# Performance work log

Measured on AMD Instinct MI355X. Metric: run time of the kernel, lower is better.

Reference implementation:

```python
import jax, jax.numpy as jnp
import numpy as np

N = 50000
E = 800000
IN_CH = 256
OUT_CH = 64   # per-head channels (PyG out_channels)
HEADS = 4
NEG_SLOPE = 0.2


def setup_inputs() -> dict:
    key = jax.random.key(0)
    k = jax.random.split(key, 8)
    x = jax.random.normal(k[0], (N, IN_CH), dtype=jnp.float32)
    edge_index = jax.random.randint(k[1], (2, E), 0, N, dtype=jnp.int64)
    # GATConv parameters
    W = jax.random.normal(k[2], (IN_CH, HEADS * OUT_CH), dtype=jnp.float32) * (1.0 / np.sqrt(IN_CH))
    att_src = jax.random.normal(k[3], (HEADS, OUT_CH), dtype=jnp.float32) * 0.1
    att_dst = jax.random.normal(k[4], (HEADS, OUT_CH), dtype=jnp.float32) * 0.1
    bias = jnp.zeros((OUT_CH,), dtype=jnp.float32)
    # residual linear (bias=False)
    W_res = jax.random.normal(k[5], (IN_CH, OUT_CH), dtype=jnp.float32) * (1.0 / np.sqrt(IN_CH))
    return {"x": x, "edge_index": edge_index, "W": W, "att_src": att_src,
            "att_dst": att_dst, "bias": bias, "W_res": W_res}


def _gat_forward(x, edge_index, W, att_src, att_dst, bias, W_res):
    # residual branch
    x_res = x @ W_res                                   # [N, OUT_CH]

    # node transform: [N, H, C]
    xw = (x @ W).reshape(N, HEADS, OUT_CH)
    # per-node attention logits, [N, H]
    a_src = jnp.einsum('nhc,hc->nh', xw, att_src)
    a_dst = jnp.einsum('nhc,hc->nh', xw, att_dst)

    # add self-loops (PyG GATConv default add_self_loops=True)
    loops = jnp.arange(N, dtype=edge_index.dtype)
    src = jnp.concatenate([edge_index[0], loops])       # [E+N]
    dst = jnp.concatenate([edge_index[1], loops])       # [E+N]

    # per-edge logits + leaky relu, [E+N, H]
    alpha = jax.nn.leaky_relu(a_src[src] + a_dst[dst], NEG_SLOPE)

    # segment softmax over destination nodes
    m = jax.ops.segment_max(alpha, dst, num_segments=N)    # [N, H]
    e = jnp.exp(alpha - m[dst])
    denom = jax.ops.segment_sum(e, dst, num_segments=N)    # [N, H]
    a = e / denom[dst]                                     # [E+N, H]
    # (dropout p=0.1 on attention coeffs is identity in eval mode)

    # weighted scatter-aggregate: [N, H, C]
    msgs = xw[src] * a[:, :, None]
    out = jax.ops.segment_sum(msgs, dst, num_segments=N)

    # concat=False -> mean over heads, then bias
    x_conv = out.mean(axis=1) + bias                     # [N, OUT_CH]
    return jax.nn.relu(x_conv + x_res)


def reference(x, edge_index, W, att_src, att_dst, bias, W_res):
    return _gat_forward(x, edge_index, W, att_src, att_dst, bias, W_res)
```

## Files before the change

### kernel.cpp

```cpp
#include <hip/hip_runtime.h>
#include <math.h>

#define N_NODES 50000
#define N_EDGES 800000
#define IN_CH   256
#define OUT_CH  64
#define HEADS   4
#define NEG_SLOPE 0.2f
#define NCOLS   320
#define NTILES  20
#define NKK     8
#define PACK_BLOCKS 40
#define GEMM_BLOCKS 782
#define SCAN_BLOCKS 196
#define NBINS   391
#define P1_BLOCKS 256
#define EPB     3125
#define AGG_BLOCKS 12500

typedef __attribute__((ext_vector_type(8))) short short8;
typedef __attribute__((ext_vector_type(4))) float f32x4;

__device__ __forceinline__ float lrelu(float v) {
    return v > 0.f ? v : NEG_SLOPE * v;
}
__device__ __forceinline__ unsigned bf16_rne(float f) {
    unsigned u = __float_as_uint(f);
    return (u + 0x7FFFu + ((u >> 16) & 1u)) >> 16;
}
__device__ __forceinline__ unsigned pack2(float lo, float hi) {
    return bf16_rne(lo) | (bf16_rne(hi) << 16);
}
__device__ __forceinline__ float bflo(unsigned u) { return __uint_as_float(u << 16); }
__device__ __forceinline__ float bfhi(unsigned u) { return __uint_as_float(u & 0xFFFF0000u); }
__device__ __forceinline__ short8 as_short8(uint4 u) {
    union { uint4 u4; short8 s8; } cv; cv.u4 = u; return cv.s8;
}

__global__ __launch_bounds__(256) void pack_B(
    const float* __restrict__ W, const float* __restrict__ Wres,
    uint4* __restrict__ Bp)
{
    const int idx  = blockIdx.x * 256 + threadIdx.x;
    const int kk   = idx / (NTILES * 64);
    const int rem  = idx - kk * (NTILES * 64);
    const int t    = rem >> 6;
    const int lane = rem & 63;
    const int colL = lane & 15, quad = lane >> 4;
    const int col  = t * 16 + colL;
    const int k0   = kk * 32 + quad * 8;
    float v[8];
    #pragma unroll
    for (int j = 0; j < 8; ++j) {
        const int k = k0 + j;
        v[j] = (col < IN_CH) ? W[(size_t)k * IN_CH + col]
                             : Wres[(size_t)k * OUT_CH + (col - IN_CH)];
    }
    uint4 u;
    u.x = pack2(v[0], v[1]); u.y = pack2(v[2], v[3]);
    u.z = pack2(v[4], v[5]); u.w = pack2(v[6], v[7]);
    Bp[(kk * NTILES + t) * 64 + lane] = u;
}

__global__ __launch_bounds__(256) void gemm_hist(
    const float* __restrict__ x, const uint4* __restrict__ Bp,
    uint2* __restrict__ xw2, float* __restrict__ xres,
    const int* __restrict__ ei, int* __restrict__ M,
    const float* __restrict__ attS, const float* __restrict__ attD,
    float* __restrict__ asrc, float* __restrict__ adst)
{
    __shared__ uint4 Alds[4 * NKK * 64];
    __shared__ float logS[64][HEADS];
    __shared__ float logD[64][HEADS];

    if (blockIdx.x >= GEMM_BLOCKS) {
        const int blk = blockIdx.x - GEMM_BLOCKS;
        int* lh = (int*)Alds;
        for (int b = threadIdx.x; b < NBINS; b += 256) lh[b] = 0;
        __syncthreads();
        const int e0 = blk * EPB;
        #pragma unroll
        for (int r = 0; r < 13; ++r) {
            const int idx = (r << 8) + threadIdx.x;
            if (idx < EPB)
                atomicAdd(&lh[ei[N_EDGES + e0 + idx] >> 7], 1);
        }
        __syncthreads();
        for (int b = threadIdx.x; b < NBINS; b += 256)
            M[(size_t)b * P1_BLOCKS + blk] = lh[b];
        return;
    }

    const int tid = threadIdx.x;
    const int n0  = blockIdx.x * 64;

    logS[tid >> 2][tid & 3] = 0.f;
    logD[tid >> 2][tid & 3] = 0.f;

    #pragma unroll
    for (int i = 0; i < 8; ++i) {
        const int e    = i * 256 + tid;
        const int g    = e >> 9;
        const int kk   = (e >> 6) & 7;
        const int lane = e & 63;
        const int cL   = lane & 15, qd = lane >> 4;
        const int row  = n0 + g * 16 + cL;
        const int k0   = kk * 32 + qd * 8;
        uint4 u = make_uint4(0u, 0u, 0u, 0u);
        if (row < N_NODES) {
            const float4 a = *reinterpret_cast<const float4*>(x + (size_t)row * IN_CH + k0);
            const float4 b = *reinterpret_cast<const float4*>(x + (size_t)row * IN_CH + k0 + 4);
            u.x = pack2(a.x, a.y); u.y = pack2(a.z, a.w);
            u.z = pack2(b.x, b.y); u.w = pack2(b.z, b.w);
        }
        Alds[(g * NKK + kk) * 64 + lane] = u;
    }
    __syncthreads();

    const int lane = tid & 63;
    const int wv   = tid >> 6;
    const int colL = lane & 15, quad = lane >> 4;

    f32x4 acc[4][5];
    #pragma unroll
    for (int rg = 0; rg < 4; ++rg)
        #pragma unroll
        for (int j = 0; j < 5; ++j) acc[rg][j] = (f32x4){0.f, 0.f, 0.f, 0.f};

    for (int kk = 0; kk < NKK; ++kk) {
        uint4 bu[5];
        #pragma unroll
        for (int j = 0; j < 5; ++j)
            bu[j] = Bp[(kk * NTILES + j * 4 + wv) * 64 + lane];
        #pragma unroll
        for (int rg = 0; rg < 4; ++rg) {
            const short8 a = as_short8(Alds[(rg * NKK + kk) * 64 + lane]);
            #pragma unroll
            for (int j = 0; j < 5; ++j)
                acc[rg][j] = __builtin_amdgcn_mfma_f32_16x16x32_bf16(
                    a, as_short8(bu[j]), acc[rg][j], 0, 0, 0);
        }
    }

    #pragma unroll
    for (int rg = 0; rg < 4; ++rg) {
        #pragma unroll
        for (int r = 0; r < 4; ++r) {
            const int row = n0 + rg * 16 + quad * 4 + r;
            if (row < N_NODES) {
                xw2[(size_t)row * 64 + wv * 16 + colL] = make_uint2(
                    pack2(acc[rg][0][r], acc[rg][1][r]),
                    pack2(acc[rg][2][r], acc[rg][3][r]));
                xres[(size_t)row * OUT_CH + wv * 16 + colL] = acc[rg][4][r];
            }
        }
    }

    float aSr[HEADS], aDr[HEADS];
    #pragma unroll
    for (int h = 0; h < HEADS; ++h) {
        aSr[h] = attS[h * 64 + wv * 16 + colL];
        aDr[h] = attD[h * 64 + wv * 16 + colL];
    }
    #pragma unroll
    for (int rg = 0; rg < 4; ++rg) {
        #pragma unroll
        for (int h = 0; h < HEADS; ++h) {
            #pragma unroll
            for (int r = 0; r < 4; ++r) {
                float vS = acc[rg][h][r] * aSr[h];
                float vD = acc[rg][h][r] * aDr[h];
                #pragma unroll
                for (int m = 1; m < 16; m <<= 1) {
                    vS += __shfl_xor(vS, m);
                    vD += __shfl_xor(vD, m);
                }
                if (colL == 0) {
                    atomicAdd(&logS[rg * 16 + quad * 4 + r][h], vS);
                    atomicAdd(&logD[rg * 16 + quad * 4 + r][h], vD);
                }
            }
        }
    }
    __syncthreads();
    {
        const int rl = tid >> 2, h = tid & 3;
        const int row = n0 + rl;
        if (row < N_NODES) {
            asrc[(size_t)row * HEADS + h] = logS[rl][h];
            adst[(size_t)row * HEADS + h] = logD[rl][h];
        }
    }
}

__global__ __launch_bounds__(256) void binscan_M(
    int* __restrict__ M, int* __restrict__ binCnt)
{
    __shared__ int ws[4];
    const int t = threadIdx.x, lane = t & 63, w = t >> 6;
    const int b = blockIdx.x;
    const int v = M[(size_t)b * P1_BLOCKS + t];
    int sc = v;
    #pragma unroll
    for (int off = 1; off < 64; off <<= 1) {
        const int n = __shfl_up(sc, off);
        if (lane >= off) sc += n;
    }
    if (lane == 63) ws[w] = sc;
    __syncthreads();
    int prefix = 0;
    for (int j = 0; j < w; ++j) prefix += ws[j];
    M[(size_t)b * P1_BLOCKS + t] = prefix + sc - v;
    if (t == 255) binCnt[b] = prefix + sc;
}

__global__ __launch_bounds__(512) void binstart_scan(
    const int* __restrict__ binCnt, int* __restrict__ binStart)
{
    __shared__ int ws[8];
    const int t = threadIdx.x, lane = t & 63, w = t >> 6;
    const int v = (t < NBINS) ? binCnt[t] : 0;
    int sc = v;
    #pragma unroll
    for (int off = 1; off < 64; off <<= 1) {
        const int n = __shfl_up(sc, off);
        if (lane >= off) sc += n;
    }
    if (lane == 63) ws[w] = sc;
    __syncthreads();
    int prefix = 0;
    for (int j = 0; j < w; ++j) prefix += ws[j];
    if (t < NBINS) binStart[t] = prefix + sc - v;
}

__global__ __launch_bounds__(256) void part_mid(
    const int* __restrict__ ei, const int* __restrict__ M,
    const int* __restrict__ binStart, unsigned* __restrict__ mid)
{
    __shared__ int baseL[NBINS];
    __shared__ int lh[NBINS];
    const int blk = blockIdx.x;
    for (int b = threadIdx.x; b < NBINS; b += 256) {
        baseL[b] = binStart[b] + M[(size_t)b * P1_BLOCKS + blk];
        lh[b] = 0;
    }
    __syncthreads();
    const int e0 = blk * EPB;
    #pragma unroll
    for (int r = 0; r < 13; ++r) {
        const int idx = (r << 8) + threadIdx.x;
        if (idx < EPB) {
            const int e = e0 + idx;
            const int d = ei[N_EDGES + e];
            const int b = d >> 7;
            const int pos = atomicAdd(&lh[b], 1);
            mid[baseL[b] + pos] = ((unsigned)(d & 127) << 17) | (unsigned)ei[e];
        }
    }
}

__global__ __launch_bounds__(256) void count_fine(
    const unsigned* __restrict__ mid, const int* __restrict__ binStart,
    const int* __restrict__ binCnt, int* __restrict__ cnt)
{
    __shared__ int c128[128];
    const int t = threadIdx.x, b = blockIdx.x;
    if (t < 128) c128[t] = 0;
    __syncthreads();
    const int base = binStart[b], n = binCnt[b];
    for (int i = t; i < n; i += 256)
        atomicAdd(&c128[mid[base + i] >> 17], 1);
    __syncthreads();
    if (t < 128) {
        const int d = (b << 7) + t;
        if (d < N_NODES) cnt[d] = c128[t];
    }
}

__global__ __launch_bounds__(256) void scan_local(
    const int* __restrict__ cnt, int* __restrict__ lscan, int* __restrict__ bsum)
{
    __shared__ int ws[4];
    const int t = threadIdx.x, lane = t & 63, w = t >> 6;
    const int i = blockIdx.x * 256 + t;
    const int v = (i < N_NODES) ? cnt[i] : 0;
    int sc = v;
    #pragma unroll
    for (int off = 1; off < 64; off <<= 1) {
        const int n = __shfl_up(sc, off);
        if (lane >= off) sc += n;
    }
    if (lane == 63) ws[w] = sc;
    __syncthreads();
    int prefix = 0;
    for (int j = 0; j < w; ++j) prefix += ws[j];
    if (i < N_NODES) lscan[i] = prefix + sc - v;
    if (t == 255) bsum[blockIdx.x] = prefix + sc;
}

__global__ __launch_bounds__(256) void scatter_fine(
    const unsigned* __restrict__ mid, const int* __restrict__ binStart,
    const int* __restrict__ binCnt, const int* __restrict__ lscan,
    const int* __restrict__ bsum, int* __restrict__ esrc)
{
    __shared__ int bsx[256];
    __shared__ int ws[4];
    __shared__ int lh[128];
    const int t = threadIdx.x, lane = t & 63, wv = t >> 6;

    const int v = (t < SCAN_BLOCKS) ? bsum[t] : 0;
    int sc = v;
    #pragma unroll
    for (int off = 1; off < 64; off <<= 1) {
        const int n = __shfl_up(sc, off);
        if (lane >= off) sc += n;
    }
    if (lane == 63) ws[wv] = sc;
    if (t < 128) lh[t] = 0;
    __syncthreads();
    int prefix = 0;
    for (int j = 0; j < wv; ++j) prefix += ws[j];
    bsx[t] = prefix + sc - v;
    __syncthreads();

    const int b = blockIdx.x;
    const int base = binStart[b], n = binCnt[b];
    for (int i = t; i < n; i += 256) {
        const unsigned m = mid[base + i];
        const int dlo = (int)(m >> 17);
        const int src = (int)(m & 0x1FFFFu);
        const int d = (b << 7) + dlo;
        const int pos = atomicAdd(&lh[dlo], 1);
        esrc[lscan[d] + bsx[d >> 8] + pos] = src;
    }
}

__global__ __launch_bounds__(256) void aggregate(
    const int* __restrict__ esrc, const int* __restrict__ lscan,
    const int* __restrict__ bsum, const int* __restrict__ cnt,
    const float* __restrict__ asrc, const float* __restrict__ adst,
    const uint2* __restrict__ xw2, const float* __restrict__ xres,
    const float* __restrict__ bias, float* __restrict__ out)
{
    __shared__ float4 wbuf[4][64];
    __shared__ int    sbuf[4][64];
    __shared__ int    bsx[256];
    __shared__ int    ws[4];
    const int t = threadIdx.x;
    const int lane = t & 63;
    const int wv   = t >> 6;

    {
        const int v = (t < SCAN_BLOCKS) ? bsum[t] : 0;
        int sc = v;
        #pragma unroll
        for (int off = 1; off < 64; off <<= 1) {
            const int n = __shfl_up(sc, off);
            if (lane >= off) sc += n;
        }
        if (lane == 63) ws[wv] = sc;
        __syncthreads();
        int prefix = 0;
        for (int j = 0; j < wv; ++j) prefix += ws[j];
        bsx[t] = prefix + sc - v;
        __syncthreads();
    }

    const int d = blockIdx.x * 4 + wv;
    const int row = lscan[d] + bsx[d >> 8];
    const int deg = cnt[d];
    const float4 ad = *reinterpret_cast<const float4*>(adst + (size_t)d * 4);
    const char* xwB = (const char*)xw2;
    const int laneB = lane << 3;

    float dn0 = 0.f, dn1 = 0.f, dn2 = 0.f, dn3 = 0.f;
    float ac0 = 0.f, ac1 = 0.f, ac2 = 0.f, ac3 = 0.f;

    for (int base = 0; base < deg; base += 64) {
        const int m = min(64, deg - base);
        if (lane < m) {
            const int s = esrc[row + base + lane];
            const float4 as = *reinterpret_cast<const float4*>(asrc + (size_t)s * 4);
            const float e0 = __expf(lrelu(as.x + ad.x));
            const float e1 = __expf(lrelu(as.y + ad.y));
            const float e2 = __expf(lrelu(as.z + ad.z));
            const float e3 = __expf(lrelu(as.w + ad.w));
            dn0 += e0; dn1 += e1; dn2 += e2; dn3 += e3;
            wbuf[wv][lane] = make_float4(e0, e1, e2, e3);
            sbuf[wv][lane] = s << 9;
        }
        int j = 0;
        for (; j + 4 <= m; j += 4) {
            uint2 v0 = *(const uint2*)(xwB + sbuf[wv][j]     + laneB);
            uint2 v1 = *(const uint2*)(xwB + sbuf[wv][j + 1] + laneB);
            uint2 v2 = *(const uint2*)(xwB + sbuf[wv][j + 2] + laneB);
            uint2 v3 = *(const uint2*)(xwB + sbuf[wv][j + 3] + laneB);
            {
                const float4 w = wbuf[wv][j];
                ac0 = fmaf(w.x, bflo(v0.x), ac0); ac1 = fmaf(w.y, bfhi(v0.x), ac1);
                ac2 = fmaf(w.z, bflo(v0.y), ac2); ac3 = fmaf(w.w, bfhi(v0.y), ac3);
            }
            {
                const float4 w = wbuf[wv][j + 1];
                ac0 = fmaf(w.x, bflo(v1.x), ac0); ac1 = fmaf(w.y, bfhi(v1.x), ac1);
                ac2 = fmaf(w.z, bflo(v1.y), ac2); ac3 = fmaf(w.w, bfhi(v1.y), ac3);
            }
            {
                const float4 w = wbuf[wv][j + 2];
                ac0 = fmaf(w.x, bflo(v2.x), ac0); ac1 = fmaf(w.y, bfhi(v2.x), ac1);
                ac2 = fmaf(w.z, bflo(v2.y), ac2); ac3 = fmaf(w.w, bfhi(v2.y), ac3);
            }
            {
                const float4 w = wbuf[wv][j + 3];
                ac0 = fmaf(w.x, bflo(v3.x), ac0); ac1 = fmaf(w.y, bfhi(v3.x), ac1);
                ac2 = fmaf(w.z, bflo(v3.y), ac2); ac3 = fmaf(w.w, bfhi(v3.y), ac3);
            }
        }
        for (; j < m; ++j) {
            const float4 w = wbuf[wv][j];
            const uint2 v = *(const uint2*)(xwB + sbuf[wv][j] + laneB);
            ac0 = fmaf(w.x, bflo(v.x), ac0);
            ac1 = fmaf(w.y, bfhi(v.x), ac1);
            ac2 = fmaf(w.z, bflo(v.y), ac2);
            ac3 = fmaf(w.w, bfhi(v.y), ac3);
        }
    }

    #pragma unroll
    for (int off = 32; off >= 1; off >>= 1) {
        dn0 += __shfl_xor(dn0, off);
        dn1 += __shfl_xor(dn1, off);
        dn2 += __shfl_xor(dn2, off);
        dn3 += __shfl_xor(dn3, off);
    }
    const float4 asd = *reinterpret_cast<const float4*>(asrc + (size_t)d * 4);
    const float s0 = __expf(lrelu(asd.x + ad.x));
    const float s1 = __expf(lrelu(asd.y + ad.y));
    const float s2 = __expf(lrelu(asd.z + ad.z));
    const float s3 = __expf(lrelu(asd.w + ad.w));
    const uint2 u = xw2[(size_t)d * 64 + lane];
    ac0 = fmaf(s0, bflo(u.x), ac0); ac1 = fmaf(s1, bfhi(u.x), ac1);
    ac2 = fmaf(s2, bflo(u.y), ac2); ac3 = fmaf(s3, bfhi(u.y), ac3);
    const float i0 = 0.25f / (dn0 + s0);
    const float i1 = 0.25f / (dn1 + s1);
    const float i2 = 0.25f / (dn2 + s2);
    const float i3 = 0.25f / (dn3 + s3);
    const float v = ac0 * i0 + ac1 * i1 + ac2 * i2 + ac3 * i3
                  + bias[lane] + xres[(size_t)d * OUT_CH + lane];
    out[(size_t)d * OUT_CH + lane] = fmaxf(v, 0.f);
}

extern "C" void kernel_launch(void* const* d_in, const int* in_sizes, int n_in,
                              void* d_out, int out_size, void* d_ws, size_t ws_size,
                              hipStream_t stream) {
    const float* x    = (const float*)d_in[0];
    const int*   ei   = (const int*)d_in[1];
    const float* W    = (const float*)d_in[2];
    const float* attS = (const float*)d_in[3];
    const float* attD = (const float*)d_in[4];
    const float* bias = (const float*)d_in[5];
    const float* Wres = (const float*)d_in[6];
    float* out = (float*)d_out;

    char* p = (char*)d_ws;
    uint4*    Bp      = (uint4*)p;    p += (size_t)NKK * NTILES * 64 * 16;
    uint2*    xw2     = (uint2*)p;    p += (size_t)N_NODES * 64 * 8;
    float*    xres    = (float*)p;    p += (size_t)N_NODES * OUT_CH * 4;
    float*    asrc    = (float*)p;    p += (size_t)N_NODES * HEADS * 4;
    float*    adst    = (float*)p;    p += (size_t)N_NODES * HEADS * 4;
    int*      M       = (int*)p;      p += (size_t)NBINS * P1_BLOCKS * 4;
    int*      binCnt  = (int*)p;      p += 512 * 4;
    int*      binStart= (int*)p;      p += 512 * 4;
    int*      cnt     = (int*)p;      p += (size_t)N_NODES * 4;
    int*      lscan   = (int*)p;      p += (size_t)N_NODES * 4;
    int*      bsum    = (int*)p;      p += 256 * 4;
    unsigned* mid     = (unsigned*)p; p += (size_t)N_EDGES * 4;
    int*      esrc    = (int*)p;      p += (size_t)N_EDGES * 4;

    pack_B<<<PACK_BLOCKS, 256, 0, stream>>>(W, Wres, Bp);
    gemm_hist<<<GEMM_BLOCKS + P1_BLOCKS, 256, 0, stream>>>(
        x, Bp, xw2, xres, ei, M, attS, attD, asrc, adst);
    binscan_M<<<NBINS, 256, 0, stream>>>(M, binCnt);
    binstart_scan<<<1, 512, 0, stream>>>(binCnt, binStart);
    part_mid<<<P1_BLOCKS, 256, 0, stream>>>(ei, M, binStart, mid);
    count_fine<<<NBINS, 256, 0, stream>>>(mid, binStart, binCnt, cnt);
    scan_local<<<SCAN_BLOCKS, 256, 0, stream>>>(cnt, lscan, bsum);
    scatter_fine<<<NBINS, 256, 0, stream>>>(mid, binStart, binCnt, lscan, bsum, esrc);
    aggregate<<<AGG_BLOCKS, 256, 0, stream>>>(
        esrc, lscan, bsum, cnt, asrc, adst, xw2, xres, bias, out);
}
```

Measured before the change: 241.0 us.

## Fuse CSR-build scans into partition and fine-scatter kernels, split aggregate launch

Folds the bin-start scan into part_mid and merges count_fine, scan_local and scatter_fine into one kernel that computes per-node offsets directly with a shared-memory stash of bin entries. This removes three kernel launches and a global re-read of the mid array, and the aggregate kernel no longer rescans block sums in every block. The aggregate launch is now split into two half-sized launches over node ranges, which adds a launch. Bins larger than the stash capacity fall back to global reads.

```diff
diff --git a/kernel.cpp b/kernel.cpp
--- a/kernel.cpp
+++ b/kernel.cpp
@@ -12,11 +12,11 @@
 #define NKK     8
 #define PACK_BLOCKS 40
 #define GEMM_BLOCKS 782
-#define SCAN_BLOCKS 196
 #define NBINS   391
 #define P1_BLOCKS 256
 #define EPB     3125
-#define AGG_BLOCKS 12500
+#define AGG_BLOCKS 6250
+#define STASH_CAP 2816
 
 typedef __attribute__((ext_vector_type(8))) short short8;
 typedef __attribute__((ext_vector_type(4))) float f32x4;
@@ -214,41 +214,65 @@
     if (t == 255) binCnt[b] = prefix + sc;
 }
 
-__global__ __launch_bounds__(512) void binstart_scan(
-    const int* __restrict__ binCnt, int* __restrict__ binStart)
-{
-    __shared__ int ws[8];
-    const int t = threadIdx.x, lane = t & 63, w = t >> 6;
-    const int v = (t < NBINS) ? binCnt[t] : 0;
-    int sc = v;
-    #pragma unroll
-    for (int off = 1; off < 64; off <<= 1) {
-        const int n = __shfl_up(sc, off);
-        if (lane >= off) sc += n;
-    }
-    if (lane == 63) ws[w] = sc;
-    __syncthreads();
-    int prefix = 0;
-    for (int j = 0; j < w; ++j) prefix += ws[j];
-    if (t < NBINS) binStart[t] = prefix + sc - v;
-}
-
 __global__ __launch_bounds__(256) void part_mid(
     const int* __restrict__ ei, const int* __restrict__ M,
-    const int* __restrict__ binStart, unsigned* __restrict__ mid)
-{
+    const int* __restrict__ binCnt, unsigned* __restrict__ mid)
+{
+    __shared__ int bc[NBINS];
+    __shared__ int bs[NBINS];
     __shared__ int baseL[NBINS];
     __shared__ int lh[NBINS];
+    __shared__ int ws[4];
+    const int t = threadIdx.x, lane = t & 63, wv = t >> 6;
     const int blk = blockIdx.x;
-    for (int b = threadIdx.x; b < NBINS; b += 256) {
-        baseL[b] = binStart[b] + M[(size_t)b * P1_BLOCKS + blk];
+
+    for (int b = t; b < NBINS; b += 256) {
+        bc[b] = binCnt[b];
+        baseL[b] = M[(size_t)b * P1_BLOCKS + blk];
         lh[b] = 0;
     }
     __syncthreads();
+
+    int tot0;
+    {
+        const int v = bc[t];
+        int sc = v;
+        #pragma unroll
+        for (int off = 1; off < 64; off <<= 1) {
+            const int n = __shfl_up(sc, off);
+            if (lane >= off) sc += n;
+        }
+        if (lane == 63) ws[wv] = sc;
+        __syncthreads();
+        int prefix = 0;
+        for (int j = 0; j < wv; ++j) prefix += ws[j];
+        bs[t] = prefix + sc - v;
+        tot0 = ws[0] + ws[1] + ws[2] + ws[3];
+        __syncthreads();
+    }
+    {
+        const int i2 = 256 + t;
+        const int v = (i2 < NBINS) ? bc[i2] : 0;
+        int sc = v;
+        #pragma unroll
+        for (int off = 1; off < 64; off <<= 1) {
+            const int n = __shfl_up(sc, off);
+            if (lane >= off) sc += n;
+        }
+        if (lane == 63) ws[wv] = sc;
+        __syncthreads();
+        int prefix = 0;
+        for (int j = 0; j < wv; ++j) prefix += ws[j];
+        if (i2 < NBINS) bs[i2] = tot0 + prefix + sc - v;
+        __syncthreads();
+    }
+    for (int b = t; b < NBINS; b += 256) baseL[b] += bs[b];
+    __syncthreads();
+
     const int e0 = blk * EPB;
     #pragma unroll
     for (int r = 0; r < 13; ++r) {
-        const int idx = (r << 8) + threadIdx.x;
+        const int idx = (r << 8) + t;
         if (idx < EPB) {
             const int e = e0 + idx;
             const int d = ei[N_EDGES + e];
@@ -259,115 +283,83 @@
     }
 }
 
-__global__ __launch_bounds__(256) void count_fine(
-    const unsigned* __restrict__ mid, const int* __restrict__ binStart,
-    const int* __restrict__ binCnt, int* __restrict__ cnt)
-{
+__global__ __launch_bounds__(256) void scatter_fine2(
+    const unsigned* __restrict__ mid, const int* __restrict__ binCnt,
+    int* __restrict__ cnt, int* __restrict__ lscan, int* __restrict__ esrc)
+{
+    __shared__ int ws[4];
     __shared__ int c128[128];
-    const int t = threadIdx.x, b = blockIdx.x;
+    __shared__ int o128[128];
+    __shared__ int w0tot;
+    __shared__ unsigned stash[STASH_CAP];
+    const int t = threadIdx.x, lane = t & 63, wv = t >> 6;
+    const int b = blockIdx.x;
+
+    int acc = 0;
+    for (int j = t; j < NBINS; j += 256)
+        if (j < b) acc += binCnt[j];
+    #pragma unroll
+    for (int off = 32; off >= 1; off >>= 1) acc += __shfl_xor(acc, off);
+    if (lane == 0) ws[wv] = acc;
     if (t < 128) c128[t] = 0;
     __syncthreads();
-    const int base = binStart[b], n = binCnt[b];
-    for (int i = t; i < n; i += 256)
-        atomicAdd(&c128[mid[base + i] >> 17], 1);
-    __syncthreads();
-    if (t < 128) {
-        const int d = (b << 7) + t;
-        if (d < N_NODES) cnt[d] = c128[t];
-    }
-}
-
-__global__ __launch_bounds__(256) void scan_local(
-    const int* __restrict__ cnt, int* __restrict__ lscan, int* __restrict__ bsum)
-{
-    __shared__ int ws[4];
-    const int t = threadIdx.x, lane = t & 63, w = t >> 6;
-    const int i = blockIdx.x * 256 + t;
-    const int v = (i < N_NODES) ? cnt[i] : 0;
-    int sc = v;
-    #pragma unroll
-    for (int off = 1; off < 64; off <<= 1) {
-        const int n = __shfl_up(sc, off);
-        if (lane >= off) sc += n;
-    }
-    if (lane == 63) ws[w] = sc;
-    __syncthreads();
-    int prefix = 0;
-    for (int j = 0; j < w; ++j) prefix += ws[j];
-    if (i < N_NODES) lscan[i] = prefix + sc - v;
-    if (t == 255) bsum[blockIdx.x] = prefix + sc;
-}
-
-__global__ __launch_bounds__(256) void scatter_fine(
-    const unsigned* __restrict__ mid, const int* __restrict__ binStart,
-    const int* __restrict__ binCnt, const int* __restrict__ lscan,
-    const int* __restrict__ bsum, int* __restrict__ esrc)
-{
-    __shared__ int bsx[256];
-    __shared__ int ws[4];
-    __shared__ int lh[128];
-    const int t = threadIdx.x, lane = t & 63, wv = t >> 6;
-
-    const int v = (t < SCAN_BLOCKS) ? bsum[t] : 0;
-    int sc = v;
-    #pragma unroll
-    for (int off = 1; off < 64; off <<= 1) {
-        const int n = __shfl_up(sc, off);
-        if (lane >= off) sc += n;
-    }
-    if (lane == 63) ws[wv] = sc;
-    if (t < 128) lh[t] = 0;
-    __syncthreads();
-    int prefix = 0;
-    for (int j = 0; j < wv; ++j) prefix += ws[j];
-    bsx[t] = prefix + sc - v;
-    __syncthreads();
-
-    const int b = blockIdx.x;
-    const int base = binStart[b], n = binCnt[b];
+    const int base = ws[0] + ws[1] + ws[2] + ws[3];
+    const int n = binCnt[b];
+
     for (int i = t; i < n; i += 256) {
         const unsigned m = mid[base + i];
+        if (i < STASH_CAP) stash[i] = m;
+        atomicAdd(&c128[m >> 17], 1);
+    }
+    __syncthreads();
+
+    if (t < 128) {
+        const int v = c128[t];
+        int sc = v;
+        #pragma unroll
+        for (int off = 1; off < 64; off <<= 1) {
+            const int nn = __shfl_up(sc, off);
+            if (lane >= off) sc += nn;
+        }
+        if (t == 63) w0tot = sc;
+        __syncthreads();
+        const int ex = sc - v + (t >= 64 ? w0tot : 0);
+        o128[t] = ex;
+        const int d = (b << 7) + t;
+        if (d < N_NODES) {
+            cnt[d] = v;
+            lscan[d] = base + ex;
+        }
+        c128[t] = 0;
+    } else {
+        __syncthreads();
+    }
+    __syncthreads();
+
+    for (int i = t; i < n; i += 256) {
+        const unsigned m = (i < STASH_CAP) ? stash[i] : mid[base + i];
         const int dlo = (int)(m >> 17);
-        const int src = (int)(m & 0x1FFFFu);
-        const int d = (b << 7) + dlo;
-        const int pos = atomicAdd(&lh[dlo], 1);
-        esrc[lscan[d] + bsx[d >> 8] + pos] = src;
+        const int pos = atomicAdd(&c128[dlo], 1);
+        esrc[base + o128[dlo] + pos] = (int)(m & 0x1FFFFu);
     }
 }
 
 __global__ __launch_bounds__(256) void aggregate(
     const int* __restrict__ esrc, const int* __restrict__ lscan,
-    const int* __restrict__ bsum, const int* __restrict__ cnt,
+    const int* __restrict__ cnt,
     const float* __restrict__ asrc, const float* __restrict__ adst,
     const uint2* __restrict__ xw2, const float* __restrict__ xres,
-    const float* __restrict__ bias, float* __restrict__ out)
+    const float* __restrict__ bias, float* __restrict__ out,
+    const int d0)
 {
     __shared__ float4 wbuf[4][64];
     __shared__ int    sbuf[4][64];
-    __shared__ int    bsx[256];
-    __shared__ int    ws[4];
     const int t = threadIdx.x;
     const int lane = t & 63;
     const int wv   = t >> 6;
 
-    {
-        const int v = (t < SCAN_BLOCKS) ? bsum[t] : 0;
-        int sc = v;
-        #pragma unroll
-        for (int off = 1; off < 64; off <<= 1) {
-            const int n = __shfl_up(sc, off);
-            if (lane >= off) sc += n;
-        }
-        if (lane == 63) ws[wv] = sc;
-        __syncthreads();
-        int prefix = 0;
-        for (int j = 0; j < wv; ++j) prefix += ws[j];
-        bsx[t] = prefix + sc - v;
-        __syncthreads();
-    }
-
-    const int d = blockIdx.x * 4 + wv;
-    const int row = lscan[d] + bsx[d >> 8];
+    const int d = d0 + blockIdx.x * 4 + wv;
+    const int row = lscan[d];
     const int deg = cnt[d];
     const float4 ad = *reinterpret_cast<const float4*>(adst + (size_t)d * 4);
     const char* xwB = (const char*)xw2;
@@ -470,10 +462,8 @@
     float*    adst    = (float*)p;    p += (size_t)N_NODES * HEADS * 4;
     int*      M       = (int*)p;      p += (size_t)NBINS * P1_BLOCKS * 4;
     int*      binCnt  = (int*)p;      p += 512 * 4;
-    int*      binStart= (int*)p;      p += 512 * 4;
     int*      cnt     = (int*)p;      p += (size_t)N_NODES * 4;
     int*      lscan   = (int*)p;      p += (size_t)N_NODES * 4;
-    int*      bsum    = (int*)p;      p += 256 * 4;
     unsigned* mid     = (unsigned*)p; p += (size_t)N_EDGES * 4;
     int*      esrc    = (int*)p;      p += (size_t)N_EDGES * 4;
 
@@ -481,11 +471,10 @@
     gemm_hist<<<GEMM_BLOCKS + P1_BLOCKS, 256, 0, stream>>>(
         x, Bp, xw2, xres, ei, M, attS, attD, asrc, adst);
     binscan_M<<<NBINS, 256, 0, stream>>>(M, binCnt);
-    binstart_scan<<<1, 512, 0, stream>>>(binCnt, binStart);
-    part_mid<<<P1_BLOCKS, 256, 0, stream>>>(ei, M, binStart, mid);
-    count_fine<<<NBINS, 256, 0, stream>>>(mid, binStart, binCnt, cnt);
-    scan_local<<<SCAN_BLOCKS, 256, 0, stream>>>(cnt, lscan, bsum);
-    scatter_fine<<<NBINS, 256, 0, stream>>>(mid, binStart, binCnt, lscan, bsum, esrc);
+    part_mid<<<P1_BLOCKS, 256, 0, stream>>>(ei, M, binCnt, mid);
+    scatter_fine2<<<NBINS, 256, 0, stream>>>(mid, binCnt, cnt, lscan, esrc);
     aggregate<<<AGG_BLOCKS, 256, 0, stream>>>(
-        esrc, lscan, bsum, cnt, asrc, adst, xw2, xres, bias, out);
-}
+        esrc, lscan, cnt, asrc, adst, xw2, xres, bias, out, 0);
+    aggregate<<<AGG_BLOCKS, 256, 0, stream>>>(
+        esrc, lscan, cnt, asrc, adst, xw2, xres, bias, out, 25000);
+}
```

Result: no change. 237.5 us (-1.5%).
